# Performance work log

Hardware: AMD Instinct MI355X
Metric: run time of the kernel (lower is better)

The kernel has to match this reference:

```python
import jax, jax.numpy as jnp
import numpy as np

HIDDEN = 2048
HEADS = 16
HEAD_DIM = HIDDEN // HEADS          # 128
HALF = HEAD_DIM // 2                # 64
LATENT = HIDDEN // 4                # 512 (compression_ratio=4)
ROPE_BASE = 10000.0


def _rope_cos_sin(seq_len):
    # LlamaRotaryEmbedding with dim=HALF
    inv_freq = 1.0 / (ROPE_BASE ** (jnp.arange(0, HALF, 2, dtype=jnp.float32) / HALF))
    t = jnp.arange(seq_len, dtype=jnp.float32)
    freqs = jnp.einsum('i,j->ij', t, inv_freq)          # [S, HALF/2]
    emb = jnp.concatenate([freqs, freqs], axis=-1)       # [S, HALF]
    cos = jnp.cos(emb)[None, :, None, :]                 # [1,S,1,HALF]
    sin = jnp.sin(emb)[None, :, None, :]
    return cos, sin


def _rotate_half(x):
    x1, x2 = jnp.split(x, 2, axis=-1)
    return jnp.concatenate([-x2, x1], axis=-1)


def _apply_rope(x, cos, sin):
    return x * cos + _rotate_half(x) * sin


def setup_inputs() -> dict:
    key = jax.random.key(0)
    ks = jax.random.split(key, 10)
    B, S = 2, 2048
    std = 0.02
    inp = {
        'x':        jax.random.normal(ks[0], (B, S, HIDDEN), jnp.float32),
        # weights stored as [in, out] (transposed torch Linear weight)
        'W_kv_d':   jax.random.normal(ks[1], (HIDDEN, LATENT), jnp.float32) * std,
        'W_q_d':    jax.random.normal(ks[2], (HIDDEN, LATENT), jnp.float32) * std,
        'W_k_u':    jax.random.normal(ks[3], (LATENT, HEADS * HALF), jnp.float32) * std,
        'W_q_u':    jax.random.normal(ks[4], (LATENT, HEADS * HALF), jnp.float32) * std,
        'W_v_u':    jax.random.normal(ks[5], (LATENT, HIDDEN), jnp.float32) * std,
        'W_rope_k': jax.random.normal(ks[6], (HIDDEN, HIDDEN // 2), jnp.float32) * std,
        'W_rope_q': jax.random.normal(ks[7], (LATENT, HIDDEN // 2), jnp.float32) * std,
        'W_o':      jax.random.normal(ks[8], (HIDDEN, HIDDEN), jnp.float32) * std,
    }
    return inp


def reference(x, W_kv_d, W_q_d, W_k_u, W_q_u, W_v_u, W_rope_k, W_rope_q, W_o):
    B, S, _ = x.shape
    kv_latent = x @ W_kv_d                      # [B,S,LATENT]
    q_latent = x @ W_q_d                        # [B,S,LATENT]

    k = (kv_latent @ W_k_u).reshape(B, S, HEADS, HALF)
    q = (q_latent @ W_q_u).reshape(B, S, HEADS, HALF)
    v = (kv_latent @ W_v_u).reshape(B, S, HEADS, HEAD_DIM)

    q_rope = (q_latent @ W_rope_q).reshape(B, S, HEADS, HALF)
    k_rope = (x @ W_rope_k).reshape(B, S, HEADS, HALF)

    cos, sin = _rope_cos_sin(S)
    k_rope = _apply_rope(k_rope, cos, sin)
    q_rope = _apply_rope(q_rope, cos, sin)

    q = jnp.concatenate([q, q_rope], axis=-1)   # [B,S,H,HEAD_DIM]
    k = jnp.concatenate([k, k_rope], axis=-1)

    scale = 1.0 / jnp.sqrt(jnp.float32(HEAD_DIM))
    scores = jnp.einsum('bqhd,bkhd->bhqk', q, k) * scale   # [B,H,S,S]
    causal = jnp.tril(jnp.ones((S, S), dtype=bool))
    scores = jnp.where(causal[None, None], scores, jnp.float32(-1e30))
    attn = jax.nn.softmax(scores, axis=-1)
    y = jnp.einsum('bhqk,bkhd->bqhd', attn, v).reshape(B, S, HIDDEN)
    return y @ W_o
```

## Files before the change

### kernel.cpp

```cpp
#include <hip/hip_runtime.h>
#include <hip/hip_bf16.h>

typedef __hip_bfloat16 bf16;
typedef __attribute__((ext_vector_type(8))) short short8;
typedef __attribute__((ext_vector_type(4))) float f32x4;

#define AS1 __attribute__((address_space(1)))
#define AS3 __attribute__((address_space(3)))

__device__ __forceinline__ void gload_lds16(const bf16* gp, bf16* lp) {
  __builtin_amdgcn_global_load_lds((const AS1 void*)gp, (AS3 void*)lp, 16, 0, 0);
}

__device__ __forceinline__ float fast_exp2(float x) {
#if __has_builtin(__builtin_amdgcn_exp2f)
  return __builtin_amdgcn_exp2f(x);
#else
  return exp2f(x);
#endif
}

__device__ __forceinline__ void store_c(bf16* C, size_t idx, float v) { C[idx] = __float2bfloat16(v); }
__device__ __forceinline__ void store_c(float* C, size_t idx, float v) { C[idx] = v; }

struct __align__(8) b16x4 { bf16 a, b, c, d; };

__global__ void cvt_f32_bf16(const float* __restrict__ in, bf16* __restrict__ out) {
  const int i = (blockIdx.x * 256 + threadIdx.x) * 4;
  const float4 v = *(const float4*)(in + i);
  out[i + 0] = __float2bfloat16(v.x);
  out[i + 1] = __float2bfloat16(v.y);
  out[i + 2] = __float2bfloat16(v.z);
  out[i + 3] = __float2bfloat16(v.w);
}

struct PrepArgs {
  const float* src[8];
  bf16* dst[8];
  int R[8], C[8], cum[8];
};

__global__ void prep_kernel(PrepArgs a) {
  __shared__ bf16 t[32][33];
  const int blk = blockIdx.x;
  int e = 0;
  while (e < 7 && blk >= a.cum[e]) ++e;
  const int lt = blk - (e ? a.cum[e - 1] : 0);
  const int R = a.R[e], C = a.C[e];
  const int tpr = C >> 5;
  const int bx = lt % tpr, by = lt / tpr;
  const float* in = a.src[e];
  bf16* out = a.dst[e];
  const int c0 = bx * 32, r0 = by * 32;
  const int tx = threadIdx.x, ty = threadIdx.y;
  for (int i = 0; i < 4; ++i)
    t[ty + 8 * i][tx] = __float2bfloat16(in[(size_t)(r0 + ty + 8 * i) * C + c0 + tx]);
  __syncthreads();
  for (int i = 0; i < 4; ++i)
    out[(size_t)(c0 + ty + 8 * i) * R + r0 + tx] = t[tx][ty + 8 * i];
}

template <typename CT, int MODE>
__global__ void gemm_bt(const bf16* __restrict__ A, int lda,
                        const bf16* __restrict__ Bt,
                        CT* __restrict__ C, bf16* __restrict__ C2, int ldc,
                        int K)
{
  __shared__ __align__(16) bf16 As[128 * 32];
  __shared__ __align__(16) bf16 Bs[128 * 32];
  const int tid  = threadIdx.x;
  const int wave = tid >> 6, lane = tid & 63;
  const int quad = lane >> 4, l16 = lane & 15;
  const int m0 = blockIdx.y * 128, n0 = blockIdx.x * 128;
  const int wm = (wave >> 1) * 64, wn = (wave & 1) * 64;

  f32x4 acc[4][4];
#pragma unroll
  for (int i = 0; i < 4; ++i)
#pragma unroll
    for (int j = 0; j < 4; ++j) acc[i][j] = (f32x4){0.f, 0.f, 0.f, 0.f};

  const int r1  = tid >> 2;
  const int ks1 = (tid & 3) * 8;

  for (int k0 = 0; k0 < K; k0 += 32) {
    gload_lds16(A  + (size_t)(m0 + r1)      * lda + k0 + ks1, &As[tid * 8]);
    gload_lds16(A  + (size_t)(m0 + r1 + 64) * lda + k0 + ks1, &As[(tid + 256) * 8]);
    gload_lds16(Bt + (size_t)(n0 + r1)      * K   + k0 + ks1, &Bs[tid * 8]);
    gload_lds16(Bt + (size_t)(n0 + r1 + 64) * K   + k0 + ks1, &Bs[(tid + 256) * 8]);
    __syncthreads();

    short8 af[4], bf_[4];
#pragma unroll
    for (int mt = 0; mt < 4; ++mt)
      af[mt] = *(const short8*)&As[(wm + mt * 16 + l16) * 32 + quad * 8];
#pragma unroll
    for (int nt = 0; nt < 4; ++nt)
      bf_[nt] = *(const short8*)&Bs[(wn + nt * 16 + l16) * 32 + quad * 8];
#pragma unroll
    for (int mt = 0; mt < 4; ++mt)
#pragma unroll
      for (int nt = 0; nt < 4; ++nt)
        acc[mt][nt] = __builtin_amdgcn_mfma_f32_16x16x32_bf16(af[mt], bf_[nt], acc[mt][nt], 0, 0, 0);
    __syncthreads();
  }

#pragma unroll
  for (int mt = 0; mt < 4; ++mt) {
    const int row = m0 + wm + mt * 16 + quad * 4;
#pragma unroll
    for (int nt = 0; nt < 4; ++nt) {
      const int cn = n0 + wn + nt * 16 + l16;
      const f32x4 v = acc[mt][nt];
      if (MODE == 0) {
#pragma unroll
        for (int r = 0; r < 4; ++r)
          store_c(C, (size_t)(row + r) * ldc + cn, v[r]);
      } else if (MODE == 4) {
        if (cn < 1024) {
#pragma unroll
          for (int r = 0; r < 4; ++r)
            store_c(C, (size_t)(row + r) * 1024 + cn, v[r]);
        } else {
          const int cn2 = cn - 1024;
          const int g = ((cn2 >> 6) << 7) + 64 + (cn2 & 63);
#pragma unroll
          for (int r = 0; r < 4; ++r)
            C2[(size_t)(row + r) * 2048 + g] = __float2bfloat16(v[r]);
        }
      }
    }
  }
}

__global__ void gemm_up_fused(const bf16* __restrict__ latcat,
                              const bf16* __restrict__ wtUP,
                              const bf16* __restrict__ wtQcat,
                              bf16* __restrict__ vT, bf16* __restrict__ kfull,
                              bf16* __restrict__ qfull)
{
  const bool is2 = (blockIdx.x >= 24);
  const bf16* A  = latcat + (is2 ? 512 : 0);
  const bf16* Bt = is2 ? wtQcat : wtUP;
  const int n0 = (is2 ? (int)blockIdx.x - 24 : (int)blockIdx.x) * 128;
  const int K = 512, lda = 1024;

  __shared__ __align__(16) bf16 As[128 * 32];
  __shared__ __align__(16) bf16 Bs[128 * 32];
  const int tid  = threadIdx.x;
  const int wave = tid >> 6, lane = tid & 63;
  const int quad = lane >> 4, l16 = lane & 15;
  const int m0 = blockIdx.y * 128;
  const int wm = (wave >> 1) * 64, wn = (wave & 1) * 64;

  f32x4 acc[4][4];
#pragma unroll
  for (int i = 0; i < 4; ++i)
#pragma unroll
    for (int j = 0; j < 4; ++j) acc[i][j] = (f32x4){0.f, 0.f, 0.f, 0.f};

  const int r1  = tid >> 2;
  const int ks1 = (tid & 3) * 8;

  for (int k0 = 0; k0 < K; k0 += 32) {
    gload_lds16(A  + (size_t)(m0 + r1)      * lda + k0 + ks1, &As[tid * 8]);
    gload_lds16(A  + (size_t)(m0 + r1 + 64) * lda + k0 + ks1, &As[(tid + 256) * 8]);
    gload_lds16(Bt + (size_t)(n0 + r1)      * K   + k0 + ks1, &Bs[tid * 8]);
    gload_lds16(Bt + (size_t)(n0 + r1 + 64) * K   + k0 + ks1, &Bs[(tid + 256) * 8]);
    __syncthreads();

    short8 af[4], bf_[4];
#pragma unroll
    for (int mt = 0; mt < 4; ++mt)
      af[mt] = *(const short8*)&As[(wm + mt * 16 + l16) * 32 + quad * 8];
#pragma unroll
    for (int nt = 0; nt < 4; ++nt)
      bf_[nt] = *(const short8*)&Bs[(wn + nt * 16 + l16) * 32 + quad * 8];
#pragma unroll
    for (int mt = 0; mt < 4; ++mt)
#pragma unroll
      for (int nt = 0; nt < 4; ++nt)
        acc[mt][nt] = __builtin_amdgcn_mfma_f32_16x16x32_bf16(af[mt], bf_[nt], acc[mt][nt], 0, 0, 0);
    __syncthreads();
  }

  if (is2) {
#pragma unroll
    for (int mt = 0; mt < 4; ++mt) {
      const int row = m0 + wm + mt * 16 + quad * 4;
#pragma unroll
      for (int nt = 0; nt < 4; ++nt) {
        const int cn = n0 + wn + nt * 16 + l16;
        const int g = (((cn >> 6) & 15) << 7) + ((cn >> 10) << 6) + (cn & 63);
        const f32x4 v = acc[mt][nt];
#pragma unroll
        for (int r = 0; r < 4; ++r)
          qfull[(size_t)(row + r) * 2048 + g] = __float2bfloat16(v[r]);
      }
    }
  } else {
#pragma unroll
    for (int mt = 0; mt < 4; ++mt) {
      const int row = m0 + wm + mt * 16 + quad * 4;
#pragma unroll
      for (int nt = 0; nt < 4; ++nt) {
        const int cn = n0 + wn + nt * 16 + l16;
        const f32x4 v = acc[mt][nt];
        if (cn < 1024) {
          const int g = ((cn >> 6) << 7) + (cn & 63);
#pragma unroll
          for (int r = 0; r < 4; ++r)
            kfull[(size_t)(row + r) * 2048 + g] = __float2bfloat16(v[r]);
        } else {
          const int cn2 = cn - 1024;
          const int bb = row >> 11, s0 = row & 2047;
          b16x4 pk;
          pk.a = __float2bfloat16(v[0]); pk.b = __float2bfloat16(v[1]);
          pk.c = __float2bfloat16(v[2]); pk.d = __float2bfloat16(v[3]);
          *(b16x4*)(vT + ((size_t)(bb * 2048 + cn2)) * 2048 + s0) = pk;
        }
      }
    }
  }
}

__global__ void rope_kernel(bf16* __restrict__ q, bf16* __restrict__ k)
{
  const int idx = blockIdx.x * 256 + threadIdx.x;
  const int i = idx & 31;
  const int h = (idx >> 5) & 15;
  const int s = (idx >> 9) & 2047;
  const int b = idx >> 20;
  const size_t off = ((size_t)(b * 2048 + s)) * 2048 + h * 128 + 64;
  const float inv = fast_exp2(-(float)i * 0.41524101186092029f);
  const float ang = (float)s * inv;
  const float cs = cosf(ang), sn = sinf(ang);
  {
    bf16* p = q + off;
    const float x1 = __bfloat162float(p[i]);
    const float x2 = __bfloat162float(p[i + 32]);
    p[i]      = __float2bfloat16(x1 * cs - x2 * sn);
    p[i + 32] = __float2bfloat16(x2 * cs + x1 * sn);
  }
  {
    bf16* p = k + off;
    const float x1 = __bfloat162float(p[i]);
    const float x2 = __bfloat162float(p[i + 32]);
    p[i]      = __float2bfloat16(x1 * cs - x2 * sn);
    p[i + 32] = __float2bfloat16(x2 * cs + x1 * sn);
  }
}

__global__ __launch_bounds__(256, 2) void attn5_kernel(
    const bf16* __restrict__ Q, const bf16* __restrict__ Kf,
    const bf16* __restrict__ VT, bf16* __restrict__ Y)
{
  __shared__ __align__(16) bf16 Ks[128][136];
  __shared__ __align__(16) bf16 VTs[128][136];
  __shared__ __align__(16) bf16 Ps[4][16][72];
  const int tid  = threadIdx.x;
  const int wave = tid >> 6, lane = tid & 63;
  const int quad = lane >> 4, l16 = lane & 15;
  const int bh = blockIdx.y;
  const size_t kqbase = ((size_t)(bh >> 4) * 2048) * 2048 + (bh & 15) * 128;
  const size_t vtbase = (size_t)bh * 128 * 2048;
  const float C2 = 0.08838834764831845f * 1.4426950408889634f;
  const float MNEG = -30.0f;

  short8 ones;
#pragma unroll
  for (int i = 0; i < 8; ++i) ones[i] = (short)0x3F80;

  const int srow = tid >> 4;
  const int scol = (tid & 15) * 8;

  for (int pi = 0; pi < 2; ++pi) {
    const int qt = pi ? (31 - blockIdx.x) : blockIdx.x;
    const int q0 = qt * 64;
    const int T = (qt >> 1) + 1;
    const int row0q = q0 + wave * 16 + quad * 4;

    short8 qf[4];
    {
      const bf16* qp = Q + kqbase + (size_t)(q0 + wave * 16 + l16) * 2048 + quad * 8;
#pragma unroll
      for (int kc = 0; kc < 4; ++kc) qf[kc] = *(const short8*)(qp + kc * 32);
    }
    f32x4 o[8];
#pragma unroll
    for (int i = 0; i < 8; ++i) o[i] = (f32x4){0, 0, 0, 0};
    f32x4 lacc = (f32x4){0, 0, 0, 0};

    short8 kg[8], vg[8];
#pragma unroll
    for (int i = 0; i < 8; ++i)
      kg[i] = *(const short8*)(Kf + kqbase + (size_t)(srow + i * 16) * 2048 + scol);
#pragma unroll
    for (int i = 0; i < 8; ++i)
      vg[i] = *(const short8*)(VT + vtbase + (size_t)(srow + i * 16) * 2048 + scol);

    for (int t = 0; t < T; ++t) {
      const int k0 = t * 128;
      __syncthreads();
#pragma unroll
      for (int i = 0; i < 8; ++i) *(short8*)&Ks[srow + i * 16][scol] = kg[i];
#pragma unroll
      for (int i = 0; i < 8; ++i) *(short8*)&VTs[srow + i * 16][scol] = vg[i];
      __syncthreads();
      if (t + 1 < T) {
        const int kn = k0 + 128;
#pragma unroll
        for (int i = 0; i < 8; ++i)
          kg[i] = *(const short8*)(Kf + kqbase + (size_t)(kn + srow + i * 16) * 2048 + scol);
#pragma unroll
        for (int i = 0; i < 8; ++i)
          vg[i] = *(const short8*)(VT + vtbase + (size_t)(srow + i * 16) * 2048 + kn + scol);
      }

      const bool h1 = (k0 < q0);
      const bool fin = (t == T - 1);

      f32x4 sf[8];
#pragma unroll
      for (int kt = 0; kt < 4; ++kt) {
        f32x4 a = (f32x4){0, 0, 0, 0};
#pragma unroll
        for (int kc = 0; kc < 4; ++kc) {
          const short8 bfr = *(const short8*)&Ks[kt * 16 + l16][kc * 32 + quad * 8];
          a = __builtin_amdgcn_mfma_f32_16x16x32_bf16(qf[kc], bfr, a, 0, 0, 0);
        }
        sf[kt] = a;
      }
      if (h1) {
#pragma unroll
        for (int kt = 4; kt < 8; ++kt) {
          f32x4 a = (f32x4){0, 0, 0, 0};
#pragma unroll
          for (int kc = 0; kc < 4; ++kc) {
            const short8 bfr = *(const short8*)&Ks[kt * 16 + l16][kc * 32 + quad * 8];
            a = __builtin_amdgcn_mfma_f32_16x16x32_bf16(qf[kc], bfr, a, 0, 0, 0);
          }
          sf[kt] = a;
        }
      }
      if (fin) {
#pragma unroll
        for (int kt = 0; kt < 4; ++kt) {
          const int col = k0 + kt * 16 + l16;
#pragma unroll
          for (int r = 0; r < 4; ++r)
            sf[kt][r] = (col > row0q + r) ? -3e38f : sf[kt][r];
        }
        if (h1) {
#pragma unroll
          for (int kt = 4; kt < 8; ++kt) {
            const int col = k0 + kt * 16 + l16;
#pragma unroll
            for (int r = 0; r < 4; ++r)
              sf[kt][r] = (col > row0q + r) ? -3e38f : sf[kt][r];
          }
        }
      }
#pragma unroll
      for (int kt = 0; kt < 4; ++kt)
#pragma unroll
        for (int r = 0; r < 4; ++r) {
          const float p = fast_exp2(__builtin_fmaf(sf[kt][r], C2, MNEG));
          Ps[wave][quad * 4 + r][kt * 16 + l16] = __float2bfloat16(p);
        }
      asm volatile("s_waitcnt lgkmcnt(0)" ::: "memory");
#pragma unroll
      for (int kc = 0; kc < 2; ++kc) {
        const short8 ap = *(const short8*)&Ps[wave][l16][kc * 32 + quad * 8];
        lacc = __builtin_amdgcn_mfma_f32_16x16x32_bf16(ap, ones, lacc, 0, 0, 0);
#pragma unroll
        for (int dt = 0; dt < 8; ++dt) {
          const short8 vb = *(const short8*)&VTs[dt * 16 + l16][kc * 32 + quad * 8];
          o[dt] = __builtin_amdgcn_mfma_f32_16x16x32_bf16(ap, vb, o[dt], 0, 0, 0);
        }
      }
      if (h1) {
        asm volatile("s_waitcnt lgkmcnt(0)" ::: "memory");
#pragma unroll
        for (int kt = 4; kt < 8; ++kt)
#pragma unroll
          for (int r = 0; r < 4; ++r) {
            const float p = fast_exp2(__builtin_fmaf(sf[kt][r], C2, MNEG));
            Ps[wave][quad * 4 + r][(kt - 4) * 16 + l16] = __float2bfloat16(p);
          }
        asm volatile("s_waitcnt lgkmcnt(0)" ::: "memory");
#pragma unroll
        for (int kc = 0; kc < 2; ++kc) {
          const short8 ap = *(const short8*)&Ps[wave][l16][kc * 32 + quad * 8];
          lacc = __builtin_amdgcn_mfma_f32_16x16x32_bf16(ap, ones, lacc, 0, 0, 0);
#pragma unroll
          for (int dt = 0; dt < 8; ++dt) {
            const short8 vb = *(const short8*)&VTs[dt * 16 + l16][64 + kc * 32 + quad * 8];
            o[dt] = __builtin_amdgcn_mfma_f32_16x16x32_bf16(ap, vb, o[dt], 0, 0, 0);
          }
        }
      }
    }

#pragma unroll
    for (int r = 0; r < 4; ++r) {
      const float inv = 1.0f / lacc[r];
#pragma unroll
      for (int dt = 0; dt < 8; ++dt)
        Y[kqbase + (size_t)(row0q + r) * 2048 + dt * 16 + l16] = __float2bfloat16(o[dt][r] * inv);
    }
  }
}

extern "C" void kernel_launch(void* const* d_in, const int* in_sizes, int n_in,
                              void* d_out, int out_size, void* d_ws, size_t ws_size,
                              hipStream_t stream)
{
  const float* x      = (const float*)d_in[0];
  const float* Wkvd   = (const float*)d_in[1];
  const float* Wqd    = (const float*)d_in[2];
  const float* Wku    = (const float*)d_in[3];
  const float* Wqu    = (const float*)d_in[4];
  const float* Wvu    = (const float*)d_in[5];
  const float* Wropek = (const float*)d_in[6];
  const float* Wropeq = (const float*)d_in[7];
  const float* Wo     = (const float*)d_in[8];

  char* ws = (char*)d_ws;
  size_t off = 0;
  auto alloc = [&](size_t elems) {
    bf16* p = (bf16*)(ws + off);
    off += ((elems * sizeof(bf16) + 255) & ~(size_t)255);
    return p;
  };
  bf16* wtX    = alloc((size_t)2048 * 2048);
  bf16* wtUP   = alloc((size_t)3072 * 512);
  bf16* wtQcat = alloc((size_t)2048 * 512);
  bf16* latcat = alloc((size_t)4096 * 1024);
  bf16* wt_o   = alloc((size_t)2048 * 2048);
  bf16* xbf    = alloc((size_t)4096 * 2048);
  bf16* qfull  = alloc((size_t)4096 * 2048);
  bf16* kfull  = alloc((size_t)4096 * 2048);
  bf16* ybuf   = (bf16*)ws;
  bf16* vT     = (bf16*)d_out;
  (void)ws_size; (void)in_sizes; (void)n_in; (void)out_size;

  cvt_f32_bf16<<<8192, 256, 0, stream>>>(x, xbf);

  PrepArgs pa;
  const float* srcs[8] = {Wkvd, Wqd, Wropek, Wku, Wvu, Wqu, Wropeq, Wo};
  bf16* dsts[8] = {wtX, wtX + (size_t)512 * 2048, wtX + (size_t)1024 * 2048,
                   wtUP, wtUP + (size_t)1024 * 512,
                   wtQcat, wtQcat + (size_t)1024 * 512, wt_o};
  const int Rs[8] = {2048, 2048, 2048, 512, 512, 512, 512, 2048};
  const int Cs[8] = {512, 512, 1024, 1024, 2048, 1024, 1024, 2048};
  int cum = 0;
  for (int e = 0; e < 8; ++e) {
    pa.src[e] = srcs[e]; pa.dst[e] = dsts[e]; pa.R[e] = Rs[e]; pa.C[e] = Cs[e];
    cum += (Rs[e] >> 5) * (Cs[e] >> 5);
    pa.cum[e] = cum;
  }
  prep_kernel<<<cum, dim3(32, 8), 0, stream>>>(pa);

  gemm_bt<bf16, 4><<<dim3(16, 32), 256, 0, stream>>>(xbf, 2048, wtX, latcat, kfull, 1024, 2048);
  gemm_up_fused<<<dim3(40, 32), 256, 0, stream>>>(latcat, wtUP, wtQcat, vT, kfull, qfull);

  rope_kernel<<<(2 * 2048 * 16 * 32) / 256, 256, 0, stream>>>(qfull, kfull);
  attn5_kernel<<<dim3(16, 32), 256, 0, stream>>>(qfull, kfull, vT, ybuf);
  gemm_bt<float, 0><<<dim3(16, 32), 256, 0, stream>>>(ybuf, 2048, wt_o, (float*)d_out, (bf16*)nullptr, 2048, 2048);
}
```

Baseline: 360.2 us.

## Split attention into one q-tile per block with 64-wide KV tiles

The attention kernel stops pairing two q-tiles per block for causal load balance and launches one block per (batch-head, q-tile), with the heaviest tiles scheduled first through a reversed blockIdx.y. KV tiles shrink from 128 to 64 keys, which roughly halves LDS use and lets launch bounds allow three blocks per CU for higher occupancy. In exchange there are more loop iterations and barriers per key, and it relies on the hardware scheduler to balance uneven causal work instead of explicit pairing.

```diff
diff --git a/kernel.cpp b/kernel.cpp
--- a/kernel.cpp
+++ b/kernel.cpp
@@ -251,17 +251,18 @@
   }
 }
 
-__global__ __launch_bounds__(256, 2) void attn5_kernel(
+__global__ __launch_bounds__(256, 3) void attn6_kernel(
     const bf16* __restrict__ Q, const bf16* __restrict__ Kf,
     const bf16* __restrict__ VT, bf16* __restrict__ Y)
 {
-  __shared__ __align__(16) bf16 Ks[128][136];
-  __shared__ __align__(16) bf16 VTs[128][136];
+  __shared__ __align__(16) bf16 Ks[64][136];
+  __shared__ __align__(16) bf16 VTs[128][72];
   __shared__ __align__(16) bf16 Ps[4][16][72];
   const int tid  = threadIdx.x;
   const int wave = tid >> 6, lane = tid & 63;
   const int quad = lane >> 4, l16 = lane & 15;
-  const int bh = blockIdx.y;
+  const int bh = blockIdx.x;
+  const int qt = 31 - blockIdx.y;
   const size_t kqbase = ((size_t)(bh >> 4) * 2048) * 2048 + (bh & 15) * 128;
   const size_t vtbase = (size_t)bh * 128 * 2048;
   const float C2 = 0.08838834764831845f * 1.4426950408889634f;
@@ -271,144 +272,96 @@
 #pragma unroll
   for (int i = 0; i < 8; ++i) ones[i] = (short)0x3F80;
 
-  const int srow = tid >> 4;
-  const int scol = (tid & 15) * 8;
-
-  for (int pi = 0; pi < 2; ++pi) {
-    const int qt = pi ? (31 - blockIdx.x) : blockIdx.x;
-    const int q0 = qt * 64;
-    const int T = (qt >> 1) + 1;
-    const int row0q = q0 + wave * 16 + quad * 4;
-
-    short8 qf[4];
-    {
-      const bf16* qp = Q + kqbase + (size_t)(q0 + wave * 16 + l16) * 2048 + quad * 8;
-#pragma unroll
-      for (int kc = 0; kc < 4; ++kc) qf[kc] = *(const short8*)(qp + kc * 32);
-    }
-    f32x4 o[8];
-#pragma unroll
-    for (int i = 0; i < 8; ++i) o[i] = (f32x4){0, 0, 0, 0};
-    f32x4 lacc = (f32x4){0, 0, 0, 0};
-
-    short8 kg[8], vg[8];
-#pragma unroll
-    for (int i = 0; i < 8; ++i)
-      kg[i] = *(const short8*)(Kf + kqbase + (size_t)(srow + i * 16) * 2048 + scol);
-#pragma unroll
-    for (int i = 0; i < 8; ++i)
-      vg[i] = *(const short8*)(VT + vtbase + (size_t)(srow + i * 16) * 2048 + scol);
-
-    for (int t = 0; t < T; ++t) {
-      const int k0 = t * 128;
-      __syncthreads();
-#pragma unroll
-      for (int i = 0; i < 8; ++i) *(short8*)&Ks[srow + i * 16][scol] = kg[i];
-#pragma unroll
-      for (int i = 0; i < 8; ++i) *(short8*)&VTs[srow + i * 16][scol] = vg[i];
-      __syncthreads();
-      if (t + 1 < T) {
-        const int kn = k0 + 128;
-#pragma unroll
-        for (int i = 0; i < 8; ++i)
-          kg[i] = *(const short8*)(Kf + kqbase + (size_t)(kn + srow + i * 16) * 2048 + scol);
-#pragma unroll
-        for (int i = 0; i < 8; ++i)
-          vg[i] = *(const short8*)(VT + vtbase + (size_t)(srow + i * 16) * 2048 + kn + scol);
-      }
-
-      const bool h1 = (k0 < q0);
-      const bool fin = (t == T - 1);
-
-      f32x4 sf[8];
+  const int krow = tid >> 4, kcol = (tid & 15) * 8;
+  const int vrow = tid >> 3, vcol = (tid & 7) * 8;
+
+  const int q0 = qt * 64;
+  const int T = qt + 1;
+  const int row0q = q0 + wave * 16 + quad * 4;
+
+  short8 qf[4];
+  {
+    const bf16* qp = Q + kqbase + (size_t)(q0 + wave * 16 + l16) * 2048 + quad * 8;
+#pragma unroll
+    for (int kc = 0; kc < 4; ++kc) qf[kc] = *(const short8*)(qp + kc * 32);
+  }
+  f32x4 o[8];
+#pragma unroll
+  for (int i = 0; i < 8; ++i) o[i] = (f32x4){0, 0, 0, 0};
+  f32x4 lacc = (f32x4){0, 0, 0, 0};
+
+  short8 kg[4], vg[4];
+#pragma unroll
+  for (int i = 0; i < 4; ++i)
+    kg[i] = *(const short8*)(Kf + kqbase + (size_t)(krow + i * 16) * 2048 + kcol);
+#pragma unroll
+  for (int i = 0; i < 4; ++i)
+    vg[i] = *(const short8*)(VT + vtbase + (size_t)(vrow + i * 32) * 2048 + vcol);
+
+  for (int t = 0; t < T; ++t) {
+    const int k0 = t * 64;
+    __syncthreads();
+#pragma unroll
+    for (int i = 0; i < 4; ++i) *(short8*)&Ks[krow + i * 16][kcol] = kg[i];
+#pragma unroll
+    for (int i = 0; i < 4; ++i) *(short8*)&VTs[vrow + i * 32][vcol] = vg[i];
+    __syncthreads();
+    if (t + 1 < T) {
+      const int kn = k0 + 64;
+#pragma unroll
+      for (int i = 0; i < 4; ++i)
+        kg[i] = *(const short8*)(Kf + kqbase + (size_t)(kn + krow + i * 16) * 2048 + kcol);
+#pragma unroll
+      for (int i = 0; i < 4; ++i)
+        vg[i] = *(const short8*)(VT + vtbase + (size_t)(vrow + i * 32) * 2048 + kn + vcol);
+    }
+
+    f32x4 sf[4];
+#pragma unroll
+    for (int kt = 0; kt < 4; ++kt) {
+      f32x4 a = (f32x4){0, 0, 0, 0};
+#pragma unroll
+      for (int kc = 0; kc < 4; ++kc) {
+        const short8 bfr = *(const short8*)&Ks[kt * 16 + l16][kc * 32 + quad * 8];
+        a = __builtin_amdgcn_mfma_f32_16x16x32_bf16(qf[kc], bfr, a, 0, 0, 0);
+      }
+      sf[kt] = a;
+    }
+    if (t == T - 1) {
 #pragma unroll
       for (int kt = 0; kt < 4; ++kt) {
-        f32x4 a = (f32x4){0, 0, 0, 0};
-#pragma unroll
-        for (int kc = 0; kc < 4; ++kc) {
-          const short8 bfr = *(const short8*)&Ks[kt * 16 + l16][kc * 32 + quad * 8];
-          a = __builtin_amdgcn_mfma_f32_16x16x32_bf16(qf[kc], bfr, a, 0, 0, 0);
-        }
-        sf[kt] = a;
-      }
-      if (h1) {
-#pragma unroll
-        for (int kt = 4; kt < 8; ++kt) {
-          f32x4 a = (f32x4){0, 0, 0, 0};
-#pragma unroll
-          for (int kc = 0; kc < 4; ++kc) {
-            const short8 bfr = *(const short8*)&Ks[kt * 16 + l16][kc * 32 + quad * 8];
-            a = __builtin_amdgcn_mfma_f32_16x16x32_bf16(qf[kc], bfr, a, 0, 0, 0);
-          }
-          sf[kt] = a;
-        }
-      }
-      if (fin) {
-#pragma unroll
-        for (int kt = 0; kt < 4; ++kt) {
-          const int col = k0 + kt * 16 + l16;
-#pragma unroll
-          for (int r = 0; r < 4; ++r)
-            sf[kt][r] = (col > row0q + r) ? -3e38f : sf[kt][r];
-        }
-        if (h1) {
-#pragma unroll
-          for (int kt = 4; kt < 8; ++kt) {
-            const int col = k0 + kt * 16 + l16;
-#pragma unroll
-            for (int r = 0; r < 4; ++r)
-              sf[kt][r] = (col > row0q + r) ? -3e38f : sf[kt][r];
-          }
-        }
-      }
-#pragma unroll
-      for (int kt = 0; kt < 4; ++kt)
-#pragma unroll
-        for (int r = 0; r < 4; ++r) {
-          const float p = fast_exp2(__builtin_fmaf(sf[kt][r], C2, MNEG));
-          Ps[wave][quad * 4 + r][kt * 16 + l16] = __float2bfloat16(p);
-        }
-      asm volatile("s_waitcnt lgkmcnt(0)" ::: "memory");
-#pragma unroll
-      for (int kc = 0; kc < 2; ++kc) {
-        const short8 ap = *(const short8*)&Ps[wave][l16][kc * 32 + quad * 8];
-        lacc = __builtin_amdgcn_mfma_f32_16x16x32_bf16(ap, ones, lacc, 0, 0, 0);
-#pragma unroll
-        for (int dt = 0; dt < 8; ++dt) {
-          const short8 vb = *(const short8*)&VTs[dt * 16 + l16][kc * 32 + quad * 8];
-          o[dt] = __builtin_amdgcn_mfma_f32_16x16x32_bf16(ap, vb, o[dt], 0, 0, 0);
-        }
-      }
-      if (h1) {
-        asm volatile("s_waitcnt lgkmcnt(0)" ::: "memory");
-#pragma unroll
-        for (int kt = 4; kt < 8; ++kt)
-#pragma unroll
-          for (int r = 0; r < 4; ++r) {
-            const float p = fast_exp2(__builtin_fmaf(sf[kt][r], C2, MNEG));
-            Ps[wave][quad * 4 + r][(kt - 4) * 16 + l16] = __float2bfloat16(p);
-          }
-        asm volatile("s_waitcnt lgkmcnt(0)" ::: "memory");
-#pragma unroll
-        for (int kc = 0; kc < 2; ++kc) {
-          const short8 ap = *(const short8*)&Ps[wave][l16][kc * 32 + quad * 8];
-          lacc = __builtin_amdgcn_mfma_f32_16x16x32_bf16(ap, ones, lacc, 0, 0, 0);
-#pragma unroll
-          for (int dt = 0; dt < 8; ++dt) {
-            const short8 vb = *(const short8*)&VTs[dt * 16 + l16][64 + kc * 32 + quad * 8];
-            o[dt] = __builtin_amdgcn_mfma_f32_16x16x32_bf16(ap, vb, o[dt], 0, 0, 0);
-          }
-        }
-      }
-    }
-
-#pragma unroll
-    for (int r = 0; r < 4; ++r) {
-      const float inv = 1.0f / lacc[r];
-#pragma unroll
-      for (int dt = 0; dt < 8; ++dt)
-        Y[kqbase + (size_t)(row0q + r) * 2048 + dt * 16 + l16] = __float2bfloat16(o[dt][r] * inv);
-    }
+        const int col = k0 + kt * 16 + l16;
+#pragma unroll
+        for (int r = 0; r < 4; ++r)
+          sf[kt][r] = (col > row0q + r) ? -3e38f : sf[kt][r];
+      }
+    }
+#pragma unroll
+    for (int kt = 0; kt < 4; ++kt)
+#pragma unroll
+      for (int r = 0; r < 4; ++r) {
+        const float p = fast_exp2(__builtin_fmaf(sf[kt][r], C2, MNEG));
+        Ps[wave][quad * 4 + r][kt * 16 + l16] = __float2bfloat16(p);
+      }
+    asm volatile("s_waitcnt lgkmcnt(0)" ::: "memory");
+#pragma unroll
+    for (int kc = 0; kc < 2; ++kc) {
+      const short8 ap = *(const short8*)&Ps[wave][l16][kc * 32 + quad * 8];
+      lacc = __builtin_amdgcn_mfma_f32_16x16x32_bf16(ap, ones, lacc, 0, 0, 0);
+#pragma unroll
+      for (int dt = 0; dt < 8; ++dt) {
+        const short8 vb = *(const short8*)&VTs[dt * 16 + l16][kc * 32 + quad * 8];
+        o[dt] = __builtin_amdgcn_mfma_f32_16x16x32_bf16(ap, vb, o[dt], 0, 0, 0);
+      }
+    }
+  }
+
+#pragma unroll
+  for (int r = 0; r < 4; ++r) {
+    const float inv = 1.0f / lacc[r];
+#pragma unroll
+    for (int dt = 0; dt < 8; ++dt)
+      Y[kqbase + (size_t)(row0q + r) * 2048 + dt * 16 + l16] = __float2bfloat16(o[dt][r] * inv);
   }
 }
 
@@ -466,6 +419,6 @@
   gemm_up_fused<<<dim3(40, 32), 256, 0, stream>>>(latcat, wtUP, wtQcat, vT, kfull, qfull);
 
   rope_kernel<<<(2 * 2048 * 16 * 32) / 256, 256, 0, stream>>>(qfull, kfull);
-  attn5_kernel<<<dim3(16, 32), 256, 0, stream>>>(qfull, kfull, vT, ybuf);
+  attn6_kernel<<<dim3(32, 32), 256, 0, stream>>>(qfull, kfull, vT, ybuf);
   gemm_bt<float, 0><<<dim3(16, 32), 256, 0, stream>>>(ybuf, 2048, wt_o, (float*)d_out, (bf16*)nullptr, 2048, 2048);
 }
```

Result: faster. 328.9 us (-8.7%).
